# Kernel optimization log

Measured on AMD Instinct MI355X. Metric: run time of the kernel, lower is better.

## Reference

```python
import jax, jax.numpy as jnp
import numpy as np

B, QLEN, MLEN, C, H = 2, 1024, 1024, 1024, 16
DK = C // H
KLEN = QLEN + MLEN


def setup_inputs() -> dict:
    key0 = jax.random.key(0)
    ks = jax.random.split(key0, 11)
    w_scale = 1.0 / np.sqrt(C)
    return {
        "key": jax.random.normal(ks[0], (B, KLEN, C), jnp.float32),
        "query": jax.random.normal(ks[1], (B, QLEN, C), jnp.float32),
        "pos_embs": jax.random.normal(ks[2], (KLEN, 1, C), jnp.float32),
        "mask": jnp.ones((B, 1, QLEN, KLEN), jnp.int32),
        "u_bias": jax.random.normal(ks[3], (H, DK), jnp.float32) * 0.02,
        "v_bias": jax.random.normal(ks[4], (H, DK), jnp.float32) * 0.02,
        "Wk": jax.random.normal(ks[5], (C, C), jnp.float32) * w_scale,
        "Wv": jax.random.normal(ks[6], (C, C), jnp.float32) * w_scale,
        "Wq": jax.random.normal(ks[7], (C, C), jnp.float32) * w_scale,
        "Wo": jax.random.normal(ks[8], (C, C), jnp.float32) * w_scale,
        "Wp": jax.random.normal(ks[9], (C, C), jnp.float32) * w_scale,
    }


def _rel_shift(x):
    # x: [B, qlen, klen, H] -> Transformer-XL pad/reshape shift trick
    b, q, k, h = x.shape
    xp = jnp.pad(x, ((0, 0), (0, 0), (1, 0), (0, 0)))       # [B, q, k+1, H]
    xp = xp.reshape(b, k + 1, q, h)[:, 1:]                   # [B, k, q, H]
    return xp.reshape(b, q, k, h)


def reference(key, query, pos_embs, mask, u_bias, v_bias, Wk, Wv, Wq, Wo, Wp):
    bs, qlen = query.shape[:2]
    klen = key.shape[1]
    n_heads, d_k = u_bias.shape
    scale = jnp.sqrt(jnp.asarray(d_k, key.dtype))

    k = (key @ Wk.T).reshape(bs, klen, n_heads, d_k)
    v = (key @ Wv.T).reshape(bs, klen, n_heads, d_k)
    # NOTE: original module projects key[:, -qlen:] (not `query`) as queries.
    q = (key[:, -qlen:] @ Wq.T).reshape(bs, qlen, n_heads, d_k)
    p = (pos_embs @ Wp.T).reshape(-1, n_heads, d_k)          # [klen, H, d_k]

    AC = jnp.einsum('bihd,bjhd->bijh', q + u_bias[None, None], k)
    BD = jnp.einsum('bihd,jhd->bijh', q + v_bias[None, None], p)
    BD = _rel_shift(BD)
    e = (AC + BD) / scale                                    # [B, q, k, H]

    m = mask[:, 0, :, :, None]                               # squeeze(1).unsqueeze(-1)
    e = jnp.where(m == 0, jnp.finfo(e.dtype).min, e)

    aw = jax.nn.softmax(e, axis=2)                           # softmax over klen
    cv = jnp.einsum('bijh,bjhd->bihd', aw, v).reshape(bs, qlen, n_heads * d_k)
    cv = cv @ Wo.T
    return cv, aw.transpose(0, 3, 1, 2)
```

## Files before the change

kernel.cpp:

```cpp
#include <hip/hip_runtime.h>
#include <hip/hip_bf16.h>


typedef __hip_bfloat16 bf16;
typedef __attribute__((ext_vector_type(8))) short bf16x8v;
typedef __attribute__((ext_vector_type(4))) float f32x4;

#define MFMA16(A, B, C) __builtin_amdgcn_mfma_f32_16x16x32_bf16(A, B, C, 0, 0, 0)

#define QL 1024
#define KL 2048
#define NH 16
#define DKD 64
#define CD 1024

static __device__ __forceinline__ unsigned short f2bf(float x) {
  __hip_bfloat16 h = __float2bfloat16(x);
  return __builtin_bit_cast(unsigned short, h);
}
static __device__ __forceinline__ float bf2f(unsigned short u) {
  return __builtin_bit_cast(float, (unsigned)u << 16);
}

typedef const __attribute__((address_space(1))) void* gptr_t;
typedef __attribute__((address_space(3))) void* sptr_t;


__global__ void cast_all(const float* __restrict__ key, const float* __restrict__ pos,
                         const float* __restrict__ wk, const float* __restrict__ wv,
                         const float* __restrict__ wq, const float* __restrict__ wp,
                         const float* __restrict__ wo,
                         bf16* __restrict__ keyb, bf16* __restrict__ qsrc,
                         bf16* __restrict__ posb, bf16* __restrict__ wkvb,
                         bf16* __restrict__ wqpb, bf16* __restrict__ wob) {
  const int bid = blockIdx.x;
  if (bid < 4096) {
    int i = (bid * 256 + threadIdx.x) * 4;
    float4 v = *(const float4*)(key + i);
    ushort4 o;
    o.x = f2bf(v.x); o.y = f2bf(v.y); o.z = f2bf(v.z); o.w = f2bf(v.w);
    *(ushort4*)((unsigned short*)keyb + i) = o;
    int row = i >> 10;
    int col = i & (CD - 1);
    int r2 = row & (KL - 1);
    if (r2 >= QL) {
      int qrow = (row >> 11) * QL + (r2 - QL);
      *(ushort4*)((unsigned short*)qsrc + (size_t)qrow * CD + col) = o;
    }
    return;
  }
  const int mb = bid - 4096;
  const float* src;
  bf16* dst;
  int cb;
  if (mb < 2048)      { src = pos; dst = posb;           cb = mb; }
  else if (mb < 3072) { src = wk;  dst = wkvb;           cb = mb - 2048; }
  else if (mb < 4096) { src = wv;  dst = wkvb + (1<<20); cb = mb - 3072; }
  else if (mb < 5120) { src = wq;  dst = wqpb;           cb = mb - 4096; }
  else if (mb < 6144) { src = wp;  dst = wqpb + (1<<20); cb = mb - 5120; }
  else                { src = wo;  dst = wob;            cb = mb - 6144; }
  int i = cb * 1024 + threadIdx.x * 4;
  float4 v = *(const float4*)(src + i);
  ushort4 o;
  o.x = f2bf(v.x); o.y = f2bf(v.y); o.z = f2bf(v.z); o.w = f2bf(v.w);
  *(ushort4*)((unsigned short*)dst + i) = o;
}


template <int MODE>
__global__ __launch_bounds__(256) void gemm_bt(
    const bf16* __restrict__ Ain, const bf16* __restrict__ A2,
    const bf16* __restrict__ Btin,
    void* __restrict__ O1, void* __restrict__ O2, void* __restrict__ O3,
    const float* __restrict__ bias1, const float* __restrict__ bias2,
    int M, int N, int K) {
  __shared__ __align__(16) bf16 As[128 * 32];
  __shared__ __align__(16) bf16 Bs[128 * 32];
  const int tid = threadIdx.x;
  const int lane = tid & 63;
  const int wid = tid >> 6;
  const int wr = wid >> 1, wc = wid & 1;
  const int lrow = lane & 15, lk = lane >> 4;
  const int m0 = blockIdx.x * 128, n0 = blockIdx.y * 128;

  const bf16* A = Ain;
  const bf16* Bt = Btin;
  if (MODE == 5) {
    if (blockIdx.z) { A = A2; Bt = Btin + (size_t)(1 << 20); }
  }

  f32x4 acc[4][4];
#pragma unroll
  for (int i = 0; i < 4; i++)
#pragma unroll
    for (int j = 0; j < 4; j++) acc[i][j] = (f32x4){0.f, 0.f, 0.f, 0.f};

  for (int k0 = 0; k0 < K; k0 += 32) {
#pragma unroll
    for (int st = 0; st < 2; ++st) {
      int c = st * 256 + tid;
      __builtin_amdgcn_global_load_lds(
          (gptr_t)(A + (size_t)(m0 + (c >> 2)) * K + k0 + (c & 3) * 8),
          (sptr_t)(As + c * 8), 16, 0, 0);
      __builtin_amdgcn_global_load_lds(
          (gptr_t)(Bt + (size_t)(n0 + (c >> 2)) * K + k0 + (c & 3) * 8),
          (sptr_t)(Bs + c * 8), 16, 0, 0);
    }
    __syncthreads();
    bf16x8v aF[4], bF[4];
#pragma unroll
    for (int s = 0; s < 4; s++) {
      aF[s] = *(const bf16x8v*)(As + (wr * 64 + s * 16 + lrow) * 32 + lk * 8);
      bF[s] = *(const bf16x8v*)(Bs + (wc * 64 + s * 16 + lrow) * 32 + lk * 8);
    }
#pragma unroll
    for (int i = 0; i < 4; i++)
#pragma unroll
      for (int j = 0; j < 4; j++) acc[i][j] = MFMA16(aF[i], bF[j], acc[i][j]);
    __syncthreads();
  }

  const int row0 = m0 + wr * 64 + lk * 4;
  const int col0 = n0 + wc * 64 + lrow;

  if (MODE == 1) {
    float* C = (float*)O1;
#pragma unroll
    for (int i = 0; i < 4; i++)
#pragma unroll
      for (int j = 0; j < 4; j++) {
        int r = row0 + i * 16, c = col0 + j * 16;
#pragma unroll
        for (int q = 0; q < 4; q++) C[(size_t)(r + q) * N + c] = acc[i][j][q];
      }
  } else if (MODE == 4) {
    if (n0 < 1024) {
      bf16* C = (bf16*)O1;
#pragma unroll
      for (int i = 0; i < 4; i++)
#pragma unroll
        for (int j = 0; j < 4; j++) {
          int c = col0 + j * 16;
          const int hh = c >> 6, dd = c & 63;
#pragma unroll
          for (int q = 0; q < 4; q++) {
            int m = row0 + i * 16 + q;
            const int bb = m >> 11, jj = m & (KL - 1);
            C[((size_t)(bb * NH + hh) * KL + jj) * DKD + dd] = __float2bfloat16(acc[i][j][q]);
          }
        }
    } else {
      unsigned short* C = (unsigned short*)O2;
#pragma unroll
      for (int i = 0; i < 4; i++)
#pragma unroll
        for (int j = 0; j < 4; j++) {
          int m = row0 + i * 16;
          int c = col0 + j * 16 - 1024;
          int bb = m >> 11;
          int jj = m & (KL - 1);
          int bhh = bb * NH + (c >> 6);
          int dd = c & (DKD - 1);
          ushort4 o;
          o.x = f2bf(acc[i][j][0]); o.y = f2bf(acc[i][j][1]);
          o.z = f2bf(acc[i][j][2]); o.w = f2bf(acc[i][j][3]);
          *(ushort4*)(C + (size_t)(bhh * DKD + dd) * KL + jj) = o;
        }
    }
  } else {
    if (blockIdx.z == 0) {
      bf16* C1 = (bf16*)O1;
      bf16* C2 = (bf16*)O2;
#pragma unroll
      for (int i = 0; i < 4; i++)
#pragma unroll
        for (int j = 0; j < 4; j++) {
          int r = row0 + i * 16, c = col0 + j * 16;
          float b1 = bias1[c], b2 = bias2[c];
#pragma unroll
          for (int q = 0; q < 4; q++) {
            float v = acc[i][j][q];
            C1[(size_t)(r + q) * CD + c] = __float2bfloat16(v + b1);
            C2[(size_t)(r + q) * CD + c] = __float2bfloat16(v + b2);
          }
        }
    } else {
      bf16* C = (bf16*)O3;
#pragma unroll
      for (int i = 0; i < 4; i++)
#pragma unroll
        for (int j = 0; j < 4; j++) {
          int r = row0 + i * 16, c = col0 + j * 16;
#pragma unroll
          for (int q = 0; q < 4; q++) C[(size_t)(r + q) * CD + c] = __float2bfloat16(acc[i][j][q]);
        }
    }
  }
}


__global__ __launch_bounds__(256) void bd_gemm(
    const bf16* __restrict__ qvb, const bf16* __restrict__ Pbuf,
    unsigned short* __restrict__ BDsh) {
  __shared__ __align__(16) bf16 As[128 * 32];
  __shared__ __align__(16) bf16 Bs[128 * 32];
  const int tid = threadIdx.x;
  const int lane = tid & 63;
  const int wid = tid >> 6;
  const int wr = wid >> 1, wc = wid & 1;
  const int lrow = lane & 15, lk = lane >> 4;
  const int m0 = blockIdx.x * 128, n0 = blockIdx.y * 128;
  const int bh = blockIdx.z, b = bh >> 4, h = bh & 15;

  const bf16* A = qvb + (size_t)(b * QL + m0) * CD + h * DKD;
  const bf16* Bt = Pbuf + (size_t)n0 * CD + h * DKD;

  f32x4 acc[4][4];
#pragma unroll
  for (int i = 0; i < 4; i++)
#pragma unroll
    for (int j = 0; j < 4; j++) acc[i][j] = (f32x4){0.f, 0.f, 0.f, 0.f};

#pragma unroll
  for (int k0 = 0; k0 < 64; k0 += 32) {
#pragma unroll
    for (int st = 0; st < 2; ++st) {
      int c = st * 256 + tid;
      __builtin_amdgcn_global_load_lds(
          (gptr_t)(A + (size_t)(c >> 2) * CD + k0 + (c & 3) * 8),
          (sptr_t)(As + c * 8), 16, 0, 0);
      __builtin_amdgcn_global_load_lds(
          (gptr_t)(Bt + (size_t)(c >> 2) * CD + k0 + (c & 3) * 8),
          (sptr_t)(Bs + c * 8), 16, 0, 0);
    }
    __syncthreads();
    bf16x8v aF[4], bF[4];
#pragma unroll
    for (int s = 0; s < 4; s++) {
      aF[s] = *(const bf16x8v*)(As + (wr * 64 + s * 16 + lrow) * 32 + lk * 8);
      bF[s] = *(const bf16x8v*)(Bs + (wc * 64 + s * 16 + lrow) * 32 + lk * 8);
    }
#pragma unroll
    for (int i = 0; i < 4; i++)
#pragma unroll
      for (int j = 0; j < 4; j++) acc[i][j] = MFMA16(aF[i], bF[j], acc[i][j]);
    __syncthreads();
  }

  unsigned short* out = BDsh + (size_t)bh * QL * KL;
  const int row0 = m0 + wr * 64 + lk * 4;
  const int col0 = n0 + wc * 64 + lrow;
#pragma unroll
  for (int i = 0; i < 4; i++)
#pragma unroll
    for (int j = 0; j < 4; j++) {
      const int cg = col0 + j * 16;
#pragma unroll
      for (int q = 0; q < 4; q++) {
        const int il = row0 + i * 16 + q;
        const int thr = 1023 - il;
        unsigned short val = f2bf(acc[i][j][q]);
        if (cg >= thr) {
          out[(size_t)il * KL + (cg - thr)] = val;
        } else if (il >= 1) {
          out[(size_t)(il - 1) * KL + il + 1025 + cg] = val;
        }
      }
    }
}


__global__ __launch_bounds__(256) void attn_fused(
    const bf16* __restrict__ qu, const unsigned short* __restrict__ Kp,
    const unsigned short* __restrict__ BDsh, const unsigned short* __restrict__ Vt,
    float* __restrict__ aw, bf16* __restrict__ cvb) {
  union SMem {
    struct { unsigned short K[2][8192]; unsigned short BD[2][2048]; } a;
    struct { unsigned short V[2][8192]; unsigned short pt[2][4][16][40]; } b;
    float cv[4][16][66];
  };
  __shared__ __align__(16) SMem sm;
  __shared__ float ssum[4][16];

  const int bid = blockIdx.x;
  const int xcd = bid & 7;
  const int kk = bid >> 3;
  const int bh = xcd * 4 + (kk >> 6);
  const int i0 = (kk & 63) * 16;
  const int b = bh >> 4, h = bh & 15;
  const int tid = threadIdx.x;
  const int lane = tid & 63, wid = tid >> 6;
  const int lrow = lane & 15, lk = lane >> 4;
  const int irow = i0 + lrow;

  const size_t qoff = (size_t)(b * QL + irow) * CD + h * DKD + lk * 8;
  const bf16x8v quF0 = *(const bf16x8v*)(qu + qoff);
  const bf16x8v quF1 = *(const bf16x8v*)(qu + qoff + 32);

  const unsigned short* Kph = Kp + (size_t)bh * KL * DKD;
  const unsigned short* BDrow = BDsh + (size_t)(bh * QL + i0) * KL;
  const unsigned short* Vth = Vt + (size_t)bh * DKD * KL;
  float* awp = aw + (size_t)(bh * QL + irow) * KL;

  ushort4 pst[32];
  float lacc = 0.f;

  auto stageA = [&](int cc, int bsel) {
#pragma unroll
    for (int st = 0; st < 4; ++st) {
      const int pos = (st * 256 + tid) * 16;
      const int krow = pos >> 7;
      const int kb = (pos & 127) ^ ((krow & 7) << 4);
      __builtin_amdgcn_global_load_lds(
          (gptr_t)(Kph + (size_t)(cc * 128 + krow) * DKD + (kb >> 1)),
          (sptr_t)((char*)sm.a.K[bsel] + pos), 16, 0, 0);
    }
    {
      const int pos = tid * 16;
      const int brow = pos >> 8;
      const int bb2 = (pos & 255) ^ ((brow & 7) << 4);
      __builtin_amdgcn_global_load_lds(
          (gptr_t)(BDrow + (size_t)brow * KL + cc * 128 + (bb2 >> 1)),
          (sptr_t)((char*)sm.a.BD[bsel] + pos), 16, 0, 0);
    }
  };

  auto stageV = [&](int cc, int bsel) {
#pragma unroll
    for (int st = 0; st < 4; ++st) {
      const int pos = (st * 256 + tid) * 16;
      const int vrow = pos >> 8;
      const int vb = (pos & 255) ^ ((vrow & 7) << 4);
      __builtin_amdgcn_global_load_lds(
          (gptr_t)(Vth + (size_t)vrow * KL + cc * 128 + (vb >> 1)),
          (sptr_t)((char*)sm.b.V[bsel] + pos), 16, 0, 0);
    }
  };

  stageA(0, 0);
#pragma unroll
  for (int c = 0; c < 16; ++c) {
    const int cur = c & 1;
    if (c < 15) {
      stageA(c + 1, cur ^ 1);
      asm volatile("s_waitcnt vmcnt(5)" ::: "memory");
    } else {
      asm volatile("s_waitcnt vmcnt(0)" ::: "memory");
    }
    __builtin_amdgcn_sched_barrier(0);
    __builtin_amdgcn_s_barrier();

    const char* Kc = (const char*)sm.a.K[cur];
    const char* BDc = (const char*)sm.a.BD[cur];
#pragma unroll
    for (int s2 = 0; s2 < 2; ++s2) {
      const int jloc = wid * 32 + s2 * 16 + lrow;
      const int sw = (jloc & 7) << 4;
      const bf16x8v kF0 = *(const bf16x8v*)(Kc + jloc * 128 + ((lk * 16) ^ sw));
      const bf16x8v kF1 = *(const bf16x8v*)(Kc + jloc * 128 + ((64 + lk * 16) ^ sw));
      f32x4 ac = (f32x4){0.f, 0.f, 0.f, 0.f};
      __builtin_amdgcn_s_setprio(1);
      ac = MFMA16(kF0, quF0, ac);
      ac = MFMA16(kF1, quF1, ac);
      __builtin_amdgcn_s_setprio(0);

      const int bdb = lrow * 256 + ((wid * 64 + s2 * 32 + lk * 8) ^ ((lrow & 7) << 4));
      const ushort4 bd4 = *(const ushort4*)(BDc + bdb);
      const unsigned short* bdp = (const unsigned short*)&bd4;
      ushort4 pb;
      unsigned short* pp = (unsigned short*)&pb;
#pragma unroll
      for (int q = 0; q < 4; ++q) {
        const int jcol = c * 128 + wid * 32 + s2 * 16 + lk * 4 + q;
        const float bd = (jcol - irow == 1025) ? 0.f : bf2f(bdp[q]);
        const float pu = __expf((ac[q] + bd) * 0.125f);
        lacc += pu;
        pp[q] = f2bf(pu);
      }
      pst[c * 2 + s2] = pb;
    }
    __builtin_amdgcn_s_barrier();
  }

  lacc += __shfl_xor(lacc, 16);
  lacc += __shfl_xor(lacc, 32);
  if (lane < 16) ssum[wid][lane] = lacc;
  __syncthreads();
  const float sc =
      1.0f / (ssum[0][lrow] + ssum[1][lrow] + ssum[2][lrow] + ssum[3][lrow]);

  f32x4 cvacc[4];
#pragma unroll
  for (int dd = 0; dd < 4; ++dd) cvacc[dd] = (f32x4){0.f, 0.f, 0.f, 0.f};

  stageV(0, 0);
#pragma unroll
  for (int c = 0; c < 16; ++c) {
    const int cur = c & 1;
    if (c < 15) {
      stageV(c + 1, cur ^ 1);
      asm volatile("s_waitcnt vmcnt(4)" ::: "memory");
    } else {
      asm volatile("s_waitcnt vmcnt(0)" ::: "memory");
    }
    __builtin_amdgcn_sched_barrier(0);
    __builtin_amdgcn_s_barrier();

#pragma unroll
    for (int s2 = 0; s2 < 2; ++s2)
      *(ushort4*)(&sm.b.pt[cur][wid][lrow][s2 * 16 + lk * 4]) = pst[c * 2 + s2];
    const bf16x8v aF = *(const bf16x8v*)(&sm.b.pt[cur][wid][lrow][lk * 8]);
    const char* Vc = (const char*)sm.b.V[cur];
    __builtin_amdgcn_s_setprio(1);
#pragma unroll
    for (int dd = 0; dd < 4; ++dd) {
      const int vr = dd * 16 + lrow;
      const bf16x8v vF =
          *(const bf16x8v*)(Vc + vr * 256 + ((wid * 64 + lk * 16) ^ ((vr & 7) << 4)));
      cvacc[dd] = MFMA16(aF, vF, cvacc[dd]);
    }
    __builtin_amdgcn_s_setprio(0);
    __builtin_amdgcn_s_barrier();
  }

#pragma unroll
  for (int dd = 0; dd < 4; ++dd)
#pragma unroll
    for (int q = 0; q < 4; ++q)
      sm.cv[wid][lk * 4 + q][dd * 16 + lrow] = cvacc[dd][q];
  __syncthreads();
#pragma unroll
  for (int t4 = 0; t4 < 4; ++t4) {
    const int idx = tid + t4 * 256;
    const int row = idx >> 6, dk = idx & 63;
    const float sinv =
        1.0f / (ssum[0][row] + ssum[1][row] + ssum[2][row] + ssum[3][row]);
    const float v = sm.cv[0][row][dk] + sm.cv[1][row][dk] + sm.cv[2][row][dk] +
                    sm.cv[3][row][dk];
    cvb[(size_t)(b * QL + i0 + row) * CD + h * DKD + dk] = __float2bfloat16(v * sinv);
  }

#pragma unroll
  for (int ii = 0; ii < 32; ++ii) {
    const int cc = ii >> 1, s2 = ii & 1;
    const unsigned short* pp = (const unsigned short*)&pst[ii];
    float4 o;
    o.x = bf2f(pp[0]) * sc;
    o.y = bf2f(pp[1]) * sc;
    o.z = bf2f(pp[2]) * sc;
    o.w = bf2f(pp[3]) * sc;
    *(float4*)(awp + cc * 128 + wid * 32 + s2 * 16 + lk * 4) = o;
  }
}


extern "C" void kernel_launch(void* const* d_in, const int* in_sizes, int n_in,
                              void* d_out, int out_size, void* d_ws, size_t ws_size,
                              hipStream_t stream) {
  const float* key = (const float*)d_in[0];
  const float* pos = (const float*)d_in[2];
  const float* ub = (const float*)d_in[4];
  const float* vb = (const float*)d_in[5];
  const float* Wk = (const float*)d_in[6];
  const float* Wv = (const float*)d_in[7];
  const float* Wq = (const float*)d_in[8];
  const float* Wo = (const float*)d_in[9];
  const float* Wp = (const float*)d_in[10];

  char* ws = (char*)d_ws;
  size_t off = 0;
  bf16* keyb = (bf16*)(ws + off); off += (size_t)4096 * 1024 * 2;
  bf16* qsrc = (bf16*)(ws + off); off += (size_t)2048 * 1024 * 2;
  bf16* posb = (bf16*)(ws + off); off += (size_t)2048 * 1024 * 2;
  bf16* wkvb = (bf16*)(ws + off); off += (size_t)2048 * 1024 * 2;
  bf16* wqpb = (bf16*)(ws + off); off += (size_t)2048 * 1024 * 2;
  bf16* wob  = (bf16*)(ws + off); off += (size_t)1024 * 1024 * 2;
  bf16* Kp   = (bf16*)(ws + off); off += (size_t)4096 * 1024 * 2;
  bf16* Vt   = (bf16*)(ws + off); off += (size_t)4096 * 1024 * 2;
  bf16* qu   = (bf16*)(ws + off); off += (size_t)2048 * 1024 * 2;
  bf16* qvb  = (bf16*)(ws + off); off += (size_t)2048 * 1024 * 2;
  bf16* Pbuf = (bf16*)(ws + off); off += (size_t)2048 * 1024 * 2;
  bf16* cvb  = (bf16*)(ws + off); off += (size_t)2048 * 1024 * 2;
  unsigned short* BDsh = (unsigned short*)(ws + off); off += (size_t)32 * QL * KL * 2;

  float* cv_out = (float*)d_out;
  float* aw_out = (float*)d_out + (size_t)2 * QL * CD;

  cast_all<<<11264, 256, 0, stream>>>(key, pos, Wk, Wv, Wq, Wp, Wo,
                                      keyb, qsrc, posb, wkvb, wqpb, wob);

  gemm_bt<4><<<dim3(32, 16), 256, 0, stream>>>(keyb, nullptr, wkvb, Kp, Vt, nullptr,
                                               nullptr, nullptr, 4096, 2048, 1024);
  gemm_bt<5><<<dim3(16, 8, 2), 256, 0, stream>>>(qsrc, posb, wqpb, qu, qvb, Pbuf,
                                                 ub, vb, 2048, 1024, 1024);

  bd_gemm<<<dim3(8, 16, 32), 256, 0, stream>>>(qvb, Pbuf, BDsh);

  attn_fused<<<2048, 256, 0, stream>>>(qu, (const unsigned short*)Kp, BDsh,
                                       (const unsigned short*)Vt, aw_out, cvb);

  gemm_bt<1><<<dim3(16, 8), 256, 0, stream>>>(cvb, nullptr, wob, cv_out, nullptr, nullptr,
                                              nullptr, nullptr, 2048, 1024, 1024);
}
```

Before: 303.3 us.

## Interleave attention-weight stores with PV loop and pre-normalize probabilities

The fp32 attention-weight writes move from a tail loop after the PV matmul into the PV chunk loop, issued as nontemporal stores so they overlap with V staging and MFMA work. Probabilities are normalized before the bf16 conversion used for PV, which removes the final division of the context vector. Shared memory becomes one manually aliased buffer with a smaller footprint. The vmcnt waits are retuned to count the extra outstanding stores, and an extra barrier is added. The cost is more memory traffic in flight during the PV loop and fragile hand-counted wait values.

```diff
diff --git a/kernel.cpp b/kernel.cpp
--- a/kernel.cpp
+++ b/kernel.cpp
@@ -274,13 +274,10 @@
     const bf16* __restrict__ qu, const unsigned short* __restrict__ Kp,
     const unsigned short* __restrict__ BDsh, const unsigned short* __restrict__ Vt,
     float* __restrict__ aw, bf16* __restrict__ cvb) {
-  union SMem {
-    struct { unsigned short K[2][8192]; unsigned short BD[2][2048]; } a;
-    struct { unsigned short V[2][8192]; unsigned short pt[2][4][16][40]; } b;
-    float cv[4][16][66];
-  };
-  __shared__ __align__(16) SMem sm;
-  __shared__ float ssum[4][16];
+  __shared__ __align__(16) char smraw[40960];
+  float* ssum = (float*)(smraw + 37888);
+  unsigned short* pt = (unsigned short*)(smraw + 32768);
+  float* cvl = (float*)smraw;
 
   const int bid = blockIdx.x;
   const int xcd = bid & 7;
@@ -313,7 +310,7 @@
       const int kb = (pos & 127) ^ ((krow & 7) << 4);
       __builtin_amdgcn_global_load_lds(
           (gptr_t)(Kph + (size_t)(cc * 128 + krow) * DKD + (kb >> 1)),
-          (sptr_t)((char*)sm.a.K[bsel] + pos), 16, 0, 0);
+          (sptr_t)(smraw + bsel * 16384 + pos), 16, 0, 0);
     }
     {
       const int pos = tid * 16;
@@ -321,7 +318,7 @@
       const int bb2 = (pos & 255) ^ ((brow & 7) << 4);
       __builtin_amdgcn_global_load_lds(
           (gptr_t)(BDrow + (size_t)brow * KL + cc * 128 + (bb2 >> 1)),
-          (sptr_t)((char*)sm.a.BD[bsel] + pos), 16, 0, 0);
+          (sptr_t)(smraw + 32768 + bsel * 4096 + pos), 16, 0, 0);
     }
   };
 
@@ -333,7 +330,7 @@
       const int vb = (pos & 255) ^ ((vrow & 7) << 4);
       __builtin_amdgcn_global_load_lds(
           (gptr_t)(Vth + (size_t)vrow * KL + cc * 128 + (vb >> 1)),
-          (sptr_t)((char*)sm.b.V[bsel] + pos), 16, 0, 0);
+          (sptr_t)(smraw + bsel * 16384 + pos), 16, 0, 0);
     }
   };
 
@@ -350,8 +347,8 @@
     __builtin_amdgcn_sched_barrier(0);
     __builtin_amdgcn_s_barrier();
 
-    const char* Kc = (const char*)sm.a.K[cur];
-    const char* BDc = (const char*)sm.a.BD[cur];
+    const char* Kc = (const char*)smraw + cur * 16384;
+    const char* BDc = (const char*)smraw + 32768 + cur * 4096;
 #pragma unroll
     for (int s2 = 0; s2 < 2; ++s2) {
       const int jloc = wid * 32 + s2 * 16 + lrow;
@@ -384,10 +381,11 @@
 
   lacc += __shfl_xor(lacc, 16);
   lacc += __shfl_xor(lacc, 32);
-  if (lane < 16) ssum[wid][lane] = lacc;
+  if (lane < 16) ssum[wid * 16 + lane] = lacc;
   __syncthreads();
-  const float sc =
-      1.0f / (ssum[0][lrow] + ssum[1][lrow] + ssum[2][lrow] + ssum[3][lrow]);
+  const float sc = 1.0f / (ssum[0 * 16 + lrow] + ssum[1 * 16 + lrow] +
+                           ssum[2 * 16 + lrow] + ssum[3 * 16 + lrow]);
+  __syncthreads();
 
   f32x4 cvacc[4];
 #pragma unroll
@@ -397,20 +395,29 @@
 #pragma unroll
   for (int c = 0; c < 16; ++c) {
     const int cur = c & 1;
-    if (c < 15) {
-      stageV(c + 1, cur ^ 1);
-      asm volatile("s_waitcnt vmcnt(4)" ::: "memory");
-    } else {
-      asm volatile("s_waitcnt vmcnt(0)" ::: "memory");
-    }
+    if (c < 15) stageV(c + 1, cur ^ 1);
+    if (c == 0)      asm volatile("s_waitcnt vmcnt(4)" ::: "memory");
+    else if (c < 15) asm volatile("s_waitcnt vmcnt(6)" ::: "memory");
+    else             asm volatile("s_waitcnt vmcnt(2)" ::: "memory");
     __builtin_amdgcn_sched_barrier(0);
     __builtin_amdgcn_s_barrier();
 
 #pragma unroll
-    for (int s2 = 0; s2 < 2; ++s2)
-      *(ushort4*)(&sm.b.pt[cur][wid][lrow][s2 * 16 + lk * 4]) = pst[c * 2 + s2];
-    const bf16x8v aF = *(const bf16x8v*)(&sm.b.pt[cur][wid][lrow][lk * 8]);
-    const char* Vc = (const char*)sm.b.V[cur];
+    for (int s2 = 0; s2 < 2; ++s2) {
+      const unsigned short* pp = (const unsigned short*)&pst[c * 2 + s2];
+      const float p0 = bf2f(pp[0]) * sc;
+      const float p1 = bf2f(pp[1]) * sc;
+      const float p2 = bf2f(pp[2]) * sc;
+      const float p3 = bf2f(pp[3]) * sc;
+      f32x4 o4 = (f32x4){p0, p1, p2, p3};
+      __builtin_nontemporal_store(
+          o4, (f32x4*)(awp + c * 128 + wid * 32 + s2 * 16 + lk * 4));
+      ushort4 pb2;
+      pb2.x = f2bf(p0); pb2.y = f2bf(p1); pb2.z = f2bf(p2); pb2.w = f2bf(p3);
+      *(ushort4*)(pt + (wid * 16 + lrow) * 40 + s2 * 16 + lk * 4) = pb2;
+    }
+    const bf16x8v aF = *(const bf16x8v*)(pt + (wid * 16 + lrow) * 40 + lk * 8);
+    const char* Vc = (const char*)smraw + cur * 16384;
     __builtin_amdgcn_s_setprio(1);
 #pragma unroll
     for (int dd = 0; dd < 4; ++dd) {
@@ -427,29 +434,15 @@
   for (int dd = 0; dd < 4; ++dd)
 #pragma unroll
     for (int q = 0; q < 4; ++q)
-      sm.cv[wid][lk * 4 + q][dd * 16 + lrow] = cvacc[dd][q];
+      cvl[((wid * 16 + lk * 4 + q) * 66) + dd * 16 + lrow] = cvacc[dd][q];
   __syncthreads();
 #pragma unroll
   for (int t4 = 0; t4 < 4; ++t4) {
     const int idx = tid + t4 * 256;
     const int row = idx >> 6, dk = idx & 63;
-    const float sinv =
-        1.0f / (ssum[0][row] + ssum[1][row] + ssum[2][row] + ssum[3][row]);
-    const float v = sm.cv[0][row][dk] + sm.cv[1][row][dk] + sm.cv[2][row][dk] +
-                    sm.cv[3][row][dk];
-    cvb[(size_t)(b * QL + i0 + row) * CD + h * DKD + dk] = __float2bfloat16(v * sinv);
-  }
-
-#pragma unroll
-  for (int ii = 0; ii < 32; ++ii) {
-    const int cc = ii >> 1, s2 = ii & 1;
-    const unsigned short* pp = (const unsigned short*)&pst[ii];
-    float4 o;
-    o.x = bf2f(pp[0]) * sc;
-    o.y = bf2f(pp[1]) * sc;
-    o.z = bf2f(pp[2]) * sc;
-    o.w = bf2f(pp[3]) * sc;
-    *(float4*)(awp + cc * 128 + wid * 32 + s2 * 16 + lk * 4) = o;
+    const float v = cvl[((0 * 16 + row) * 66) + dk] + cvl[((1 * 16 + row) * 66) + dk] +
+                    cvl[((2 * 16 + row) * 66) + dk] + cvl[((3 * 16 + row) * 66) + dk];
+    cvb[(size_t)(b * QL + i0 + row) * CD + h * DKD + dk] = __float2bfloat16(v);
   }
 }
 
```

Measured after the change: 263.3 us (median of 2 runs). 13.2% less time.
